# Kernel tuning notes

Hardware: AMD Instinct MI355X
Metric: run time of the kernel (lower is better)

The kernel has to match this reference:

```python
import jax, jax.numpy as jnp
import numpy as np

DT = 0.001  # fixed dt in SimplifiedSSM.forward
LN_EPS = 1e-5


def _layernorm(x, g, b):
    m = jnp.mean(x, axis=-1, keepdims=True)
    v = jnp.mean(jnp.square(x - m), axis=-1, keepdims=True)
    return (x - m) * jax.lax.rsqrt(v + LN_EPS) * g + b


def setup_inputs() -> dict:
    key = jax.random.key(0)
    ks = jax.random.split(key, 12)
    Bn, C, H, W = 8, 1024, 32, 32
    depth, S = 4, 128
    d = C
    inp = {
        "x": jax.random.normal(ks[0], (Bn, C, H, W), dtype=jnp.float32),
        # SSM params, stacked over depth. A scaled by 0.1 for numerical stability
        # of the length-1024 recurrence (same math, tamer eigenvalues).
        "A": 0.1 * jax.random.normal(ks[1], (depth, S, S), dtype=jnp.float32),
        "Bp": jax.random.normal(ks[2], (depth, S, d), dtype=jnp.float32),
        "Cp": jax.random.normal(ks[3], (depth, d, S), dtype=jnp.float32),
        "Dp": jax.random.normal(ks[4], (depth, d), dtype=jnp.float32),
        # Linear layers (PyTorch convention: y = x @ W.T + b)
        "Wi": jax.random.normal(ks[5], (depth, d, d), dtype=jnp.float32) / np.sqrt(d),
        "bi": jax.random.normal(ks[6], (depth, d), dtype=jnp.float32) * 0.01,
        "Wo": jax.random.normal(ks[7], (depth, d, d), dtype=jnp.float32) / np.sqrt(d),
        "bo": jax.random.normal(ks[8], (depth, d), dtype=jnp.float32) * 0.01,
        # LayerNorm affine params
        "gamma": jnp.ones((depth, d), dtype=jnp.float32),
        "beta": jnp.zeros((depth, d), dtype=jnp.float32),
    }
    return inp


def reference(x, A, Bp, Cp, Dp, Wi, bi, Wo, bo, gamma, beta):
    Bn, C, H, W = x.shape
    depth, S, _ = A.shape
    # b c h w -> b (h w) c
    seq = x.reshape(Bn, C, H * W).transpose(0, 2, 1)
    eye = jnp.eye(S, dtype=x.dtype)
    for i in range(depth):
        n = _layernorm(seq, gamma[i], beta[i])
        u = n @ Wi[i].T + bi[i]                       # (B, L, d)
        A_bar = eye + DT * A[i]                       # (S, S)
        ub = jnp.einsum('bld,sd->lbs', u, DT * Bp[i]) # (L, B, S)

        def step(h, ub_t):
            h = h @ A_bar.T + ub_t
            return h, h

        h0 = jnp.zeros((Bn, S), dtype=x.dtype)
        _, hs = jax.lax.scan(step, h0, ub)            # hs: (L, B, S)
        y = jnp.einsum('lbs,ds->bld', hs, Cp[i]) + u * Dp[i]
        seq = seq + y @ Wo[i].T + bo[i]
    return seq.transpose(0, 2, 1).reshape(Bn, C, H, W)
```

## Files before the change

### kernel.cpp

```cpp
#include <hip/hip_runtime.h>
#include <stdint.h>

#define DT_STEP 0.001f
#define LN_EPS  1e-5f
#define Bn      8
#define Lseq    1024
#define Dm      1024
#define Sn      128
#define DEPTH   4
#define Mrows   (Bn * Lseq)
#define Qc      32
#define NCHUNK  (Lseq / Qc)
#define NPOW    33

typedef short bf16x8 __attribute__((ext_vector_type(8)));
typedef float f32x4  __attribute__((ext_vector_type(4)));

__device__ __forceinline__ unsigned short f2bf(float f) {
    unsigned int u = __float_as_uint(f);
    u += 0x7fffu + ((u >> 16) & 1u);
    return (unsigned short)(u >> 16);
}

#define GLOAD_LDS16(gp, lp)                                                \
    __builtin_amdgcn_global_load_lds(                                      \
        (const __attribute__((address_space(1))) unsigned int*)(gp),       \
        (__attribute__((address_space(3))) unsigned int*)(lp), 16, 0, 0)

__global__ __launch_bounds__(256) void f2bf_kernel(const float* __restrict__ src,
                                                   unsigned short* __restrict__ dst,
                                                   int n) {
    int i = (blockIdx.x * 256 + threadIdx.x) * 4;
    if (i < n) {
        float4 v = *(const float4*)(src + i);
        ushort4 o;
        o.x = f2bf(v.x); o.y = f2bf(v.y); o.z = f2bf(v.z); o.w = f2bf(v.w);
        *(ushort4*)(dst + i) = o;
    }
}

__global__ __launch_bounds__(256) void convscale_kernel(const float* __restrict__ Wo,
                                                        const float* __restrict__ Dp,
                                                        unsigned short* __restrict__ dst) {
    int z = blockIdx.y;
    int i = (blockIdx.x * 256 + threadIdx.x) * 4;
    const float* S = Wo + (size_t)z * Dm * Dm;
    const float* dp = Dp + (size_t)z * Dm;
    float4 v = *(const float4*)(S + i);
    int c = i & (Dm - 1);
    float4 d = *(const float4*)(dp + c);
    ushort4 o;
    o.x = f2bf(v.x * d.x); o.y = f2bf(v.y * d.y);
    o.z = f2bf(v.z * d.z); o.w = f2bf(v.w * d.w);
    *(ushort4*)(dst + (size_t)z * Dm * Dm + i) = o;
}

__global__ __launch_bounds__(256) void transpose_f2bf(const float* __restrict__ src,
                                                      unsigned short* __restrict__ dst,
                                                      int R, int C) {
    __shared__ float t[32][33];
    int z = blockIdx.z;
    const float* S = src + (size_t)z * R * C;
    unsigned short* D = dst + (size_t)z * R * C;
    int r0 = blockIdx.y * 32, c0 = blockIdx.x * 32;
    int tx = threadIdx.x & 31, ty = threadIdx.x >> 5;
    for (int rr = ty; rr < 32; rr += 8)
        t[rr][tx] = S[(size_t)(r0 + rr) * C + c0 + tx];
    __syncthreads();
    for (int rr = ty; rr < 32; rr += 8)
        D[(size_t)(c0 + rr) * R + r0 + tx] = f2bf(t[tx][rr]);
}

__global__ __launch_bounds__(256) void c2dt_kernel(const float* __restrict__ Bp,
                                                   const float* __restrict__ bi,
                                                   float* __restrict__ c2dt) {
    int z = blockIdx.x, s = blockIdx.y;
    int tid = threadIdx.x;
    const float* br = Bp + ((size_t)z * Sn + s) * Dm;
    const float* bb = bi + (size_t)z * Dm;
    float4 v = *(const float4*)(br + tid * 4);
    float4 w = *(const float4*)(bb + tid * 4);
    float acc = v.x * w.x + v.y * w.y + v.z * w.z + v.w * w.w;
#pragma unroll
    for (int off = 32; off > 0; off >>= 1) acc += __shfl_down(acc, off, 64);
    __shared__ float red[4];
    if ((tid & 63) == 0) red[tid >> 6] = acc;
    __syncthreads();
    if (tid == 0) c2dt[z * Sn + s] = DT_STEP * (red[0] + red[1] + red[2] + red[3]);
}

__global__ __launch_bounds__(1024) void transpose_bll(const float* __restrict__ src,
                                                      float* __restrict__ dst) {
    __shared__ float tile[32][33];
    int b  = blockIdx.z;
    int i0 = blockIdx.y * 32, j0 = blockIdx.x * 32;
    int tx = threadIdx.x, ty = threadIdx.y;
    const float* S = src + (size_t)b * Dm * Lseq;
    float*       D = dst + (size_t)b * Dm * Lseq;
    tile[ty][tx] = S[(size_t)(j0 + ty) * 1024 + i0 + tx];
    __syncthreads();
    D[(size_t)(i0 + ty) * 1024 + j0 + tx] = tile[tx][ty];
}

__global__ __launch_bounds__(256) void ln_kernel(const float* __restrict__ x,
                                                 unsigned short* __restrict__ outp,
                                                 const float* __restrict__ g,
                                                 const float* __restrict__ bta) {
    int row = blockIdx.x;
    int tid = threadIdx.x;
    const float* xr = x + (size_t)row * Dm;
    float4 v = *(const float4*)(xr + tid * 4);
    float s  = v.x + v.y + v.z + v.w;
    float ss = v.x * v.x + v.y * v.y + v.z * v.z + v.w * v.w;
#pragma unroll
    for (int off = 32; off > 0; off >>= 1) {
        s  += __shfl_down(s, off, 64);
        ss += __shfl_down(ss, off, 64);
    }
    __shared__ float red[8];
    __shared__ float mv[2];
    int wave = tid >> 6, lane = tid & 63;
    if (lane == 0) { red[wave] = s; red[4 + wave] = ss; }
    __syncthreads();
    if (tid == 0) {
        float st  = red[0] + red[1] + red[2] + red[3];
        float sst = red[4] + red[5] + red[6] + red[7];
        float mean = st / (float)Dm;
        float var  = sst / (float)Dm - mean * mean;
        mv[0] = mean;
        mv[1] = rsqrtf(var + LN_EPS);
    }
    __syncthreads();
    float mean = mv[0], rstd = mv[1];
    int c = tid * 4;
    float4 gv = *(const float4*)(g + c);
    float4 bv = *(const float4*)(bta + c);
    ushort4 o;
    o.x = f2bf((v.x - mean) * rstd * gv.x + bv.x);
    o.y = f2bf((v.y - mean) * rstd * gv.y + bv.y);
    o.z = f2bf((v.z - mean) * rstd * gv.z + bv.z);
    o.w = f2bf((v.w - mean) * rstd * gv.w + bv.w);
    *(ushort4*)(outp + (size_t)row * Dm + c) = o;
}

__global__ __launch_bounds__(256) void gemm_bk64(
    const unsigned short* __restrict__ A1, int sA1,
    const unsigned short* __restrict__ A2, int sA2, int KA1,
    const unsigned short* __restrict__ B1, int sB1,
    const unsigned short* __restrict__ B2, int sB2,
    float* __restrict__ Cf, unsigned short* __restrict__ Ch,
    const float* __restrict__ bias1, const float* __restrict__ bias2,
    int ny, int N, int K, float scale, int mode,
    long batchA, long batchB, long batchC) {
    __shared__ __align__(16) unsigned short As[1024 * 8];
    __shared__ __align__(16) unsigned short Bs[1024 * 8];
    int flat = blockIdx.x;
    int rb = flat % ny, cb = flat / ny;
    int row0 = rb * 128, col0 = cb * 128;
    int z = blockIdx.y;
    int tid  = threadIdx.x;
    int wave = tid >> 6, lane = tid & 63;
    int wm = (wave >> 1) * 64, wn = (wave & 1) * 64;
    int lr = lane & 15, lq = lane >> 4;

    int rowS[4], kclS[4];
    unsigned short *Asl[4], *Bsl[4];
#pragma unroll
    for (int q = 0; q < 4; q++) {
        int s = tid + q * 256;
        rowS[q] = s >> 3;
        kclS[q] = (s & 7) ^ ((s >> 3) & 7);
        Asl[q] = &As[s * 8];
        Bsl[q] = &Bs[s * 8];
    }
    int aoff[4][2], boff[4][2];
#pragma unroll
    for (int i = 0; i < 4; i++)
#pragma unroll
        for (int h = 0; h < 2; h++) {
            int ra = wm + i * 16 + lr;
            aoff[i][h] = (ra * 8 + ((lq + 4 * h) ^ (ra & 7))) * 8;
            int rn = wn + i * 16 + lr;
            boff[i][h] = (rn * 8 + ((lq + 4 * h) ^ (rn & 7))) * 8;
        }

    const unsigned short* A1b = A1 + (size_t)z * batchA;
    const unsigned short* BfixBlk = nullptr;
    int sBfix = sB1;
    if (mode == 0) {
        if (col0 < N - 128) { BfixBlk = B1 + (size_t)col0 * sB1; sBfix = sB1; }
        else                { BfixBlk = B2;                      sBfix = sB2; }
    } else if (mode == 2) {
        BfixBlk = B1 + (size_t)z * batchB + (size_t)col0 * sB1;
        sBfix = sB1;
    }

    f32x4 acc[4][4];
#pragma unroll
    for (int i = 0; i < 4; i++)
#pragma unroll
        for (int j = 0; j < 4; j++) acc[i][j] = (f32x4){0.f, 0.f, 0.f, 0.f};

    for (int k0 = 0; k0 < K; k0 += 64) {
        const unsigned short *Ab, *Bb;
        int sa, sb, ko;
        if (mode == 1) {
            if (k0 < KA1) { Ab = A1; sa = sA1; Bb = B1 + (size_t)col0 * sB1; sb = sB1; ko = k0; }
            else          { Ab = A2; sa = sA2; Bb = B2 + (size_t)col0 * sB2; sb = sB2; ko = k0 - KA1; }
        } else {
            Ab = A1b; sa = sA1; Bb = BfixBlk; sb = sBfix; ko = k0;
        }
        const unsigned short* Abr = Ab + (size_t)row0 * sa + ko;
        const unsigned short* Bbr = Bb + ko;
        __syncthreads();
#pragma unroll
        for (int q = 0; q < 4; q++) {
            GLOAD_LDS16(Abr + (size_t)rowS[q] * sa + kclS[q] * 8, Asl[q]);
            GLOAD_LDS16(Bbr + (size_t)rowS[q] * sb + kclS[q] * 8, Bsl[q]);
        }
        __syncthreads();
#pragma unroll
        for (int h = 0; h < 2; h++) {
            bf16x8 af[4], bfr[4];
#pragma unroll
            for (int i = 0; i < 4; i++) af[i]  = *(const bf16x8*)&As[aoff[i][h]];
#pragma unroll
            for (int j = 0; j < 4; j++) bfr[j] = *(const bf16x8*)&Bs[boff[j][h]];
#pragma unroll
            for (int i = 0; i < 4; i++)
#pragma unroll
                for (int j = 0; j < 4; j++)
                    acc[i][j] = __builtin_amdgcn_mfma_f32_16x16x32_bf16(af[i], bfr[j],
                                                                       acc[i][j], 0, 0, 0);
        }
    }
#pragma unroll
    for (int i = 0; i < 4; i++) {
#pragma unroll
        for (int j = 0; j < 4; j++) {
#pragma unroll
            for (int r = 0; r < 4; r++) {
                int row = row0 + wm + i * 16 + lq * 4 + r;
                int col = col0 + wn + j * 16 + lr;
                float v = acc[i][j][r];
                if (mode == 0) {
                    int nu = N - 128;
                    if (col < nu) {
                        Ch[(size_t)row * nu + col] = f2bf(v + bias1[col]);
                    } else {
                        int cc = col - nu;
                        Cf[(size_t)row * 128 + cc] = v + bias2[cc];
                    }
                } else if (mode == 1) {
                    size_t idx = (size_t)row * N + col;
                    Cf[idx] = Cf[idx] + v + bias1[col];
                } else {
                    Ch[(size_t)z * batchC + (size_t)row * N + col] = f2bf(v * scale);
                }
            }
        }
    }
}

__global__ __launch_bounds__(128) void pow_init(const float* __restrict__ Amat,
                                                float* __restrict__ Pow) {
    int i = blockIdx.x;
    int s = blockIdx.y;
    int k = threadIdx.x;
    float eye = (s == k) ? 1.f : 0.f;
    size_t base = (size_t)i * NPOW * (Sn * Sn);
    Pow[base + (size_t)s * Sn + k] = eye;
    Pow[base + (size_t)(Sn * Sn) + (size_t)s * Sn + k] =
        eye + DT_STEP * Amat[(size_t)i * Sn * Sn + (size_t)s * Sn + k];
}

__global__ __launch_bounds__(256) void pow_mul(float* __restrict__ Pow, int m, int kmax) {
    int job = blockIdx.z;
    int i  = job / kmax;
    int kk = job % kmax + 1;
    const float* Pa = Pow + ((size_t)i * NPOW + m) * (Sn * Sn);
    const float* Pb = Pow + ((size_t)i * NPOW + kk) * (Sn * Sn);
    float*       Pc = Pow + ((size_t)i * NPOW + m + kk) * (Sn * Sn);
    int r0 = blockIdx.y * 64, c0 = blockIdx.x * 32;
    __shared__ float Asl[64 * 129];
    __shared__ float Bsl[128 * 32];
    int tx = threadIdx.x, ty = threadIdx.y;
    int tid = ty * 16 + tx;
    for (int idx = tid; idx < 64 * 128; idx += 256) {
        int r = idx >> 7, cc = idx & 127;
        Asl[r * 129 + cc] = Pa[(size_t)(r0 + r) * 128 + cc];
    }
    for (int idx = tid; idx < 128 * 32; idx += 256) {
        int r = idx >> 5, cc = idx & 31;
        Bsl[r * 32 + cc] = Pb[(size_t)r * 128 + c0 + cc];
    }
    __syncthreads();
    float acc[4][2] = {{0.f,0.f},{0.f,0.f},{0.f,0.f},{0.f,0.f}};
    for (int k = 0; k < 128; k++) {
        float b0 = Bsl[k * 32 + tx * 2];
        float b1 = Bsl[k * 32 + tx * 2 + 1];
#pragma unroll
        for (int r = 0; r < 4; r++) {
            float a = Asl[(ty * 4 + r) * 129 + k];
            acc[r][0] += a * b0;
            acc[r][1] += a * b1;
        }
    }
#pragma unroll
    for (int r = 0; r < 4; r++) {
        Pc[(size_t)(r0 + ty * 4 + r) * 128 + c0 + tx * 2]     = acc[r][0];
        Pc[(size_t)(r0 + ty * 4 + r) * 128 + c0 + tx * 2 + 1] = acc[r][1];
    }
}

__global__ __launch_bounds__(128) void local_scan(const float* __restrict__ ub,
                                                  float* __restrict__ hs,
                                                  const float* __restrict__ Abar) {
    int b = blockIdx.x / NCHUNK;
    int c = blockIdx.x % NCHUNK;
    int s = threadIdx.x;
    float arow[Sn];
#pragma unroll
    for (int k = 0; k < Sn; k += 4) {
        float4 v = *(const float4*)(Abar + (size_t)s * Sn + k);
        arow[k] = v.x; arow[k + 1] = v.y; arow[k + 2] = v.z; arow[k + 3] = v.w;
    }
    __shared__ __align__(16) float hsh[Sn];
    hsh[s] = 0.f;
    __syncthreads();
    size_t base = (size_t)(b * Lseq + c * Qc) * Sn + s;
    for (int t = 0; t < Qc; t++) {
        float ut = ub[base + (size_t)t * Sn];
        float a0 = 0.f, a1 = 0.f, a2 = 0.f, a3 = 0.f;
#pragma unroll
        for (int k = 0; k < Sn; k += 16) {
            float4 h0 = *(const float4*)&hsh[k];
            float4 h1 = *(const float4*)&hsh[k + 4];
            float4 h2 = *(const float4*)&hsh[k + 8];
            float4 h3 = *(const float4*)&hsh[k + 12];
            a0 += arow[k + 0] * h0.x + arow[k + 1] * h0.y + arow[k + 2] * h0.z + arow[k + 3] * h0.w;
            a1 += arow[k + 4] * h1.x + arow[k + 5] * h1.y + arow[k + 6] * h1.z + arow[k + 7] * h1.w;
            a2 += arow[k + 8] * h2.x + arow[k + 9] * h2.y + arow[k + 10] * h2.z + arow[k + 11] * h2.w;
            a3 += arow[k + 12] * h3.x + arow[k + 13] * h3.y + arow[k + 14] * h3.z + arow[k + 15] * h3.w;
        }
        float hv = ut + (a0 + a1) + (a2 + a3);
        hs[base + (size_t)t * Sn] = hv;
        __syncthreads();
        hsh[s] = hv;
        __syncthreads();
    }
}

__global__ __launch_bounds__(128) void carry_scan(const float* __restrict__ hs,
                                                  const float* __restrict__ AQ,
                                                  float* __restrict__ carry) {
    int b = blockIdx.x;
    int s = threadIdx.x;
    float le[NCHUNK];
#pragma unroll
    for (int c = 0; c < NCHUNK; c++)
        le[c] = hs[(size_t)(b * Lseq + c * Qc + Qc - 1) * Sn + s];
    float arow[Sn];
#pragma unroll
    for (int k = 0; k < Sn; k += 4) {
        float4 v = *(const float4*)(AQ + (size_t)s * Sn + k);
        arow[k] = v.x; arow[k + 1] = v.y; arow[k + 2] = v.z; arow[k + 3] = v.w;
    }
    __shared__ __align__(16) float csh[Sn];
    csh[s] = 0.f;
    __syncthreads();
    for (int c = 0; c < NCHUNK; c++) {
        carry[((size_t)b * NCHUNK + c) * Sn + s] = csh[s];
        float a0 = 0.f, a1 = 0.f, a2 = 0.f, a3 = 0.f;
#pragma unroll
        for (int k = 0; k < Sn; k += 16) {
            float4 h0 = *(const float4*)&csh[k];
            float4 h1 = *(const float4*)&csh[k + 4];
            float4 h2 = *(const float4*)&csh[k + 8];
            float4 h3 = *(const float4*)&csh[k + 12];
            a0 += arow[k + 0] * h0.x + arow[k + 1] * h0.y + arow[k + 2] * h0.z + arow[k + 3] * h0.w;
            a1 += arow[k + 4] * h1.x + arow[k + 5] * h1.y + arow[k + 6] * h1.z + arow[k + 7] * h1.w;
            a2 += arow[k + 8] * h2.x + arow[k + 9] * h2.y + arow[k + 10] * h2.z + arow[k + 11] * h2.w;
            a3 += arow[k + 12] * h3.x + arow[k + 13] * h3.y + arow[k + 14] * h3.z + arow[k + 15] * h3.w;
        }
        float cv = le[c] + (a0 + a1) + (a2 + a3);
        __syncthreads();
        csh[s] = cv;
        __syncthreads();
    }
}

__global__ __launch_bounds__(256) void fixup_scan(const float* __restrict__ hs,
                                                  unsigned short* __restrict__ hs_bf,
                                                  const float* __restrict__ PowLayer,
                                                  const float* __restrict__ carry) {
    int t = blockIdx.x;
    int c = blockIdx.y;
    const float* P = PowLayer + (size_t)(t + 1) * (Sn * Sn);
    __shared__ float Pl[Sn * 65];
    __shared__ float cl[Bn * Sn];
    int tid = threadIdx.x;
    for (int idx = tid; idx < Bn * Sn; idx += 256)
        cl[idx] = carry[((size_t)(idx >> 7) * NCHUNK + c) * Sn + (idx & 127)];
    int s = tid & 127, bh = tid >> 7;
    float acc[4] = {0.f, 0.f, 0.f, 0.f};
    for (int kh = 0; kh < 2; kh++) {
        __syncthreads();
        for (int idx = tid; idx < Sn * 64; idx += 256) {
            int r = idx >> 6, kk = idx & 63;
            Pl[r * 65 + kk] = P[(size_t)r * Sn + kh * 64 + kk];
        }
        __syncthreads();
        for (int kk = 0; kk < 64; kk++) {
            float pw = Pl[s * 65 + kk];
            int kg = kh * 64 + kk;
#pragma unroll
            for (int j = 0; j < 4; j++)
                acc[j] += pw * cl[(bh * 4 + j) * Sn + kg];
        }
    }
#pragma unroll
    for (int j = 0; j < 4; j++) {
        int bb = bh * 4 + j;
        size_t rowi = (size_t)(bb * Lseq + c * Qc + t) * Sn + s;
        hs_bf[rowi] = f2bf(hs[rowi] + acc[j]);
    }
}

extern "C" void kernel_launch(void* const* d_in, const int* in_sizes, int n_in,
                              void* d_out, int out_size, void* d_ws, size_t ws_size,
                              hipStream_t stream) {
    const float* x     = (const float*)d_in[0];
    const float* Am    = (const float*)d_in[1];
    const float* Bp    = (const float*)d_in[2];
    const float* Cp    = (const float*)d_in[3];
    const float* Dp    = (const float*)d_in[4];
    const float* Wi    = (const float*)d_in[5];
    const float* bi    = (const float*)d_in[6];
    const float* Wo    = (const float*)d_in[7];
    const float* bo    = (const float*)d_in[8];
    const float* gamma = (const float*)d_in[9];
    const float* beta  = (const float*)d_in[10];
    float* out = (float*)d_out;
    (void)in_sizes; (void)n_in; (void)out_size; (void)ws_size;

    char* ws = (char*)d_ws;
    float*          seq   = (float*)(ws + (size_t)0);
    unsigned short* nbuf  = (unsigned short*)(ws + (size_t)33554432);
    unsigned short* WiTh  = (unsigned short*)(ws + (size_t)33554432);
    unsigned short* Woh   = (unsigned short*)(ws + (size_t)41943040);
    unsigned short* u     = (unsigned short*)(ws + (size_t)50331648);
    float*          ub    = (float*)(ws + (size_t)67108864);
    float*          hs    = (float*)(ws + (size_t)71303168);
    unsigned short* hs_bf = (unsigned short*)(ws + (size_t)75497472);
    float*          Pow   = (float*)(ws + (size_t)77594624);
    float*          carry = (float*)(ws + (size_t)86245376);
    unsigned short* Wih   = (unsigned short*)(ws + (size_t)86376448);
    unsigned short* Wo2h  = (unsigned short*)(ws + (size_t)94765056);
    unsigned short* Bph   = (unsigned short*)(ws + (size_t)103153664);
    unsigned short* CpTh  = (unsigned short*)(ws + (size_t)104202240);
    unsigned short* M2h   = (unsigned short*)(ws + (size_t)105250816);
    unsigned short* W3h   = (unsigned short*)(ws + (size_t)106299392);
    float*          c2dt  = (float*)(ws + (size_t)107347968);

    const long WW = (long)Dm * Dm;
    const long SW = (long)Sn * Dm;

    hipLaunchKernelGGL(f2bf_kernel, dim3(DEPTH * WW / 1024), dim3(256), 0, stream,
                       Wi, Wih, DEPTH * (int)WW);
    hipLaunchKernelGGL(f2bf_kernel, dim3(DEPTH * WW / 1024), dim3(256), 0, stream,
                       Wo, Woh, DEPTH * (int)WW);
    hipLaunchKernelGGL(f2bf_kernel, dim3(DEPTH * SW / 1024), dim3(256), 0, stream,
                       Bp, Bph, DEPTH * (int)SW);
    hipLaunchKernelGGL(convscale_kernel, dim3(WW / 1024, DEPTH), dim3(256), 0, stream,
                       Wo, Dp, Wo2h);
    hipLaunchKernelGGL(transpose_f2bf, dim3(32, 32, DEPTH), dim3(256), 0, stream,
                       Wi, WiTh, Dm, Dm);
    hipLaunchKernelGGL(transpose_f2bf, dim3(4, 32, DEPTH), dim3(256), 0, stream,
                       Cp, CpTh, Dm, Sn);
    hipLaunchKernelGGL(c2dt_kernel, dim3(DEPTH, Sn), dim3(256), 0, stream, Bp, bi, c2dt);

    hipLaunchKernelGGL(gemm_bk64, dim3(8, DEPTH), dim3(256), 0, stream,
                       Bph, Dm, (const unsigned short*)nullptr, 0, 0,
                       WiTh, Dm, (const unsigned short*)nullptr, 0,
                       (float*)nullptr, M2h, (const float*)nullptr, (const float*)nullptr,
                       1, Dm, Dm, DT_STEP, 2, SW, WW, SW);
    hipLaunchKernelGGL(gemm_bk64, dim3(8, DEPTH), dim3(256), 0, stream,
                       Woh, Dm, (const unsigned short*)nullptr, 0, 0,
                       CpTh, Dm, (const unsigned short*)nullptr, 0,
                       (float*)nullptr, W3h, (const float*)nullptr, (const float*)nullptr,
                       8, Sn, Dm, 1.f, 2, WW, SW, SW);

    hipLaunchKernelGGL(transpose_bll, dim3(32, 32, Bn), dim3(32, 32), 0, stream, x, seq);

    hipLaunchKernelGGL(pow_init, dim3(DEPTH, Sn), dim3(Sn), 0, stream, Am, Pow);
    for (int m = 1; m < Qc; m <<= 1) {
        hipLaunchKernelGGL(pow_mul, dim3(4, 2, DEPTH * m), dim3(16, 16), 0, stream,
                           Pow, m, m);
    }

    for (int i = 0; i < DEPTH; i++) {
        const unsigned short* Wi_i  = Wih  + (size_t)i * WW;
        const unsigned short* Wo2_i = Wo2h + (size_t)i * WW;
        const unsigned short* M2_i  = M2h  + (size_t)i * SW;
        const unsigned short* W3_i  = W3h  + (size_t)i * SW;
        const float* PowL = Pow + (size_t)i * NPOW * (Sn * Sn);

        hipLaunchKernelGGL(ln_kernel, dim3(Mrows), dim3(256), 0, stream,
                           seq, nbuf, gamma + i * Dm, beta + i * Dm);
        hipLaunchKernelGGL(gemm_bk64, dim3(9 * 64, 1), dim3(256), 0, stream,
                           nbuf, Dm, (const unsigned short*)nullptr, 0, 0,
                           Wi_i, Dm, M2_i, Dm,
                           ub, u, bi + i * Dm, c2dt + i * Sn,
                           64, Dm + Sn, Dm, 1.f, 0, 0, 0, 0);
        hipLaunchKernelGGL(local_scan, dim3(Bn * NCHUNK), dim3(Sn), 0, stream,
                           ub, hs, PowL + (size_t)1 * Sn * Sn);
        hipLaunchKernelGGL(carry_scan, dim3(Bn), dim3(Sn), 0, stream,
                           hs, PowL + (size_t)Qc * Sn * Sn, carry);
        hipLaunchKernelGGL(fixup_scan, dim3(Qc, NCHUNK), dim3(256), 0, stream,
                           hs, hs_bf, PowL, carry);
        hipLaunchKernelGGL(gemm_bk64, dim3(8 * 64, 1), dim3(256), 0, stream,
                           hs_bf, Sn, u, Dm, Sn,
                           W3_i, Sn, Wo2_i, Dm,
                           seq, (unsigned short*)nullptr, bo + i * Dm, (const float*)nullptr,
                           64, Dm, Dm + Sn, 1.f, 1, 0, 0, 0);
    }

    hipLaunchKernelGGL(transpose_bll, dim3(32, 32, Bn), dim3(32, 32), 0, stream, seq, out);
}
```

Measured before the change: 855.1 us.

## Double-buffer LDS tiles in bf16 GEMM to overlap global loads with MFMA

Doubles the shared-memory A/B tile buffers and restructures the K loop so the next tile's global-to-LDS loads are issued before computing on the current tile. Explicit s_waitcnt vmcnt/lgkmcnt plus s_barrier inline asm replace the two __syncthreads per iteration. The goal is to hide global memory latency behind the matrix-core work. In exchange, LDS use doubles to 64KB per block, which may reduce occupancy, and correctness now relies on hand-counted wait counts.

Result: slower. 952.2 us (+11.4%).

```diff
diff --git a/kernel.cpp b/kernel.cpp
--- a/kernel.cpp
+++ b/kernel.cpp
@@ -152,8 +152,8 @@
     const float* __restrict__ bias1, const float* __restrict__ bias2,
     int ny, int N, int K, float scale, int mode,
     long batchA, long batchB, long batchC) {
-    __shared__ __align__(16) unsigned short As[1024 * 8];
-    __shared__ __align__(16) unsigned short Bs[1024 * 8];
+    __shared__ __align__(16) unsigned short As[2][1024 * 8];
+    __shared__ __align__(16) unsigned short Bs[2][1024 * 8];
     int flat = blockIdx.x;
     int rb = flat % ny, cb = flat / ny;
     int row0 = rb * 128, col0 = cb * 128;
@@ -163,15 +163,13 @@
     int wm = (wave >> 1) * 64, wn = (wave & 1) * 64;
     int lr = lane & 15, lq = lane >> 4;
 
-    int rowS[4], kclS[4];
-    unsigned short *Asl[4], *Bsl[4];
+    int rowS[4], kclS[4], slotOff[4];
 #pragma unroll
     for (int q = 0; q < 4; q++) {
         int s = tid + q * 256;
         rowS[q] = s >> 3;
         kclS[q] = (s & 7) ^ ((s >> 3) & 7);
-        Asl[q] = &As[s * 8];
-        Bsl[q] = &Bs[s * 8];
+        slotOff[q] = s * 8;
     }
     int aoff[4][2], boff[4][2];
 #pragma unroll
@@ -195,13 +193,8 @@
         sBfix = sB1;
     }
 
-    f32x4 acc[4][4];
-#pragma unroll
-    for (int i = 0; i < 4; i++)
-#pragma unroll
-        for (int j = 0; j < 4; j++) acc[i][j] = (f32x4){0.f, 0.f, 0.f, 0.f};
-
-    for (int k0 = 0; k0 < K; k0 += 64) {
+    auto issue = [&](int kt, int buf) {
+        int k0 = kt * 64;
         const unsigned short *Ab, *Bb;
         int sa, sb, ko;
         if (mode == 1) {
@@ -212,20 +205,27 @@
         }
         const unsigned short* Abr = Ab + (size_t)row0 * sa + ko;
         const unsigned short* Bbr = Bb + ko;
-        __syncthreads();
 #pragma unroll
         for (int q = 0; q < 4; q++) {
-            GLOAD_LDS16(Abr + (size_t)rowS[q] * sa + kclS[q] * 8, Asl[q]);
-            GLOAD_LDS16(Bbr + (size_t)rowS[q] * sb + kclS[q] * 8, Bsl[q]);
-        }
-        __syncthreads();
+            GLOAD_LDS16(Abr + (size_t)rowS[q] * sa + kclS[q] * 8, &As[buf][slotOff[q]]);
+            GLOAD_LDS16(Bbr + (size_t)rowS[q] * sb + kclS[q] * 8, &Bs[buf][slotOff[q]]);
+        }
+    };
+
+    f32x4 acc[4][4];
+#pragma unroll
+    for (int i = 0; i < 4; i++)
+#pragma unroll
+        for (int j = 0; j < 4; j++) acc[i][j] = (f32x4){0.f, 0.f, 0.f, 0.f};
+
+    auto compute = [&](int buf) {
 #pragma unroll
         for (int h = 0; h < 2; h++) {
             bf16x8 af[4], bfr[4];
 #pragma unroll
-            for (int i = 0; i < 4; i++) af[i]  = *(const bf16x8*)&As[aoff[i][h]];
-#pragma unroll
-            for (int j = 0; j < 4; j++) bfr[j] = *(const bf16x8*)&Bs[boff[j][h]];
+            for (int i = 0; i < 4; i++) af[i]  = *(const bf16x8*)&As[buf][aoff[i][h]];
+#pragma unroll
+            for (int j = 0; j < 4; j++) bfr[j] = *(const bf16x8*)&Bs[buf][boff[j][h]];
 #pragma unroll
             for (int i = 0; i < 4; i++)
 #pragma unroll
@@ -233,7 +233,20 @@
                     acc[i][j] = __builtin_amdgcn_mfma_f32_16x16x32_bf16(af[i], bfr[j],
                                                                        acc[i][j], 0, 0, 0);
         }
-    }
+    };
+
+    int niter = K >> 6;
+    issue(0, 0);
+    int it = 0;
+    for (; it + 1 < niter; it++) {
+        issue(it + 1, (it + 1) & 1);
+        asm volatile("s_waitcnt vmcnt(8)\n\ts_barrier" ::: "memory");
+        compute(it & 1);
+        asm volatile("s_waitcnt lgkmcnt(0)\n\ts_barrier" ::: "memory");
+    }
+    asm volatile("s_waitcnt vmcnt(0)\n\ts_barrier" ::: "memory");
+    compute(it & 1);
+
 #pragma unroll
     for (int i = 0; i < 4; i++) {
 #pragma unroll
```

## Use 8-wave GEMM blocks and batch four chunks per fixup_scan block

Applied to the files above, without the earlier changes.

The 128x128 GEMM tile is now computed by 512 threads (8 waves, each 64x32) instead of 256 threads (4 waves, each 64x64). This halves per-thread accumulators and loads to raise latency hiding and occupancy, at the cost of more B-fragment LDS reads per MFMA. Separately, fixup_scan now handles four chunks per block, so each loaded power-matrix tile in LDS is reused across four carries, cutting redundant P loads. It quarters that kernel's block count and uses more shared memory per block.

Measured after the change: 812.2 us. -5.0%, faster.

```diff
diff --git a/kernel.cpp b/kernel.cpp
--- a/kernel.cpp
+++ b/kernel.cpp
@@ -143,7 +143,7 @@
     *(ushort4*)(outp + (size_t)row * Dm + c) = o;
 }
 
-__global__ __launch_bounds__(256) void gemm_bk64(
+__global__ __launch_bounds__(512) void gemm_bk64(
     const unsigned short* __restrict__ A1, int sA1,
     const unsigned short* __restrict__ A2, int sA2, int KA1,
     const unsigned short* __restrict__ B1, int sB1,
@@ -160,28 +160,31 @@
     int z = blockIdx.y;
     int tid  = threadIdx.x;
     int wave = tid >> 6, lane = tid & 63;
-    int wm = (wave >> 1) * 64, wn = (wave & 1) * 64;
+    int wm = (wave & 1) * 64, wn = (wave >> 1) * 32;
     int lr = lane & 15, lq = lane >> 4;
 
-    int rowS[4], kclS[4];
-    unsigned short *Asl[4], *Bsl[4];
-#pragma unroll
-    for (int q = 0; q < 4; q++) {
-        int s = tid + q * 256;
+    int rowS[2], kclS[2], slotOff[2];
+#pragma unroll
+    for (int q = 0; q < 2; q++) {
+        int s = tid + q * 512;
         rowS[q] = s >> 3;
         kclS[q] = (s & 7) ^ ((s >> 3) & 7);
-        Asl[q] = &As[s * 8];
-        Bsl[q] = &Bs[s * 8];
-    }
-    int aoff[4][2], boff[4][2];
+        slotOff[q] = s * 8;
+    }
+    int aoff[4][2], boff[2][2];
 #pragma unroll
     for (int i = 0; i < 4; i++)
 #pragma unroll
         for (int h = 0; h < 2; h++) {
             int ra = wm + i * 16 + lr;
             aoff[i][h] = (ra * 8 + ((lq + 4 * h) ^ (ra & 7))) * 8;
-            int rn = wn + i * 16 + lr;
-            boff[i][h] = (rn * 8 + ((lq + 4 * h) ^ (rn & 7))) * 8;
+        }
+#pragma unroll
+    for (int j = 0; j < 2; j++)
+#pragma unroll
+        for (int h = 0; h < 2; h++) {
+            int rn = wn + j * 16 + lr;
+            boff[j][h] = (rn * 8 + ((lq + 4 * h) ^ (rn & 7))) * 8;
         }
 
     const unsigned short* A1b = A1 + (size_t)z * batchA;
@@ -195,11 +198,11 @@
         sBfix = sB1;
     }
 
-    f32x4 acc[4][4];
+    f32x4 acc[4][2];
 #pragma unroll
     for (int i = 0; i < 4; i++)
 #pragma unroll
-        for (int j = 0; j < 4; j++) acc[i][j] = (f32x4){0.f, 0.f, 0.f, 0.f};
+        for (int j = 0; j < 2; j++) acc[i][j] = (f32x4){0.f, 0.f, 0.f, 0.f};
 
     for (int k0 = 0; k0 < K; k0 += 64) {
         const unsigned short *Ab, *Bb;
@@ -214,22 +217,22 @@
         const unsigned short* Bbr = Bb + ko;
         __syncthreads();
 #pragma unroll
-        for (int q = 0; q < 4; q++) {
-            GLOAD_LDS16(Abr + (size_t)rowS[q] * sa + kclS[q] * 8, Asl[q]);
-            GLOAD_LDS16(Bbr + (size_t)rowS[q] * sb + kclS[q] * 8, Bsl[q]);
+        for (int q = 0; q < 2; q++) {
+            GLOAD_LDS16(Abr + (size_t)rowS[q] * sa + kclS[q] * 8, &As[slotOff[q]]);
+            GLOAD_LDS16(Bbr + (size_t)rowS[q] * sb + kclS[q] * 8, &Bs[slotOff[q]]);
         }
         __syncthreads();
 #pragma unroll
         for (int h = 0; h < 2; h++) {
-            bf16x8 af[4], bfr[4];
+            bf16x8 af[4], bfr[2];
 #pragma unroll
             for (int i = 0; i < 4; i++) af[i]  = *(const bf16x8*)&As[aoff[i][h]];
 #pragma unroll
-            for (int j = 0; j < 4; j++) bfr[j] = *(const bf16x8*)&Bs[boff[j][h]];
+            for (int j = 0; j < 2; j++) bfr[j] = *(const bf16x8*)&Bs[boff[j][h]];
 #pragma unroll
             for (int i = 0; i < 4; i++)
 #pragma unroll
-                for (int j = 0; j < 4; j++)
+                for (int j = 0; j < 2; j++)
                     acc[i][j] = __builtin_amdgcn_mfma_f32_16x16x32_bf16(af[i], bfr[j],
                                                                        acc[i][j], 0, 0, 0);
         }
@@ -237,7 +240,7 @@
 #pragma unroll
     for (int i = 0; i < 4; i++) {
 #pragma unroll
-        for (int j = 0; j < 4; j++) {
+        for (int j = 0; j < 2; j++) {
 #pragma unroll
             for (int r = 0; r < 4; r++) {
                 int row = row0 + wm + i * 16 + lq * 4 + r;
@@ -394,16 +397,22 @@
                                                   unsigned short* __restrict__ hs_bf,
                                                   const float* __restrict__ PowLayer,
                                                   const float* __restrict__ carry) {
-    int t = blockIdx.x;
-    int c = blockIdx.y;
+    int t  = blockIdx.x;
+    int c4 = blockIdx.y;
     const float* P = PowLayer + (size_t)(t + 1) * (Sn * Sn);
     __shared__ float Pl[Sn * 65];
-    __shared__ float cl[Bn * Sn];
+    __shared__ float cl[4][Bn * Sn];
     int tid = threadIdx.x;
-    for (int idx = tid; idx < Bn * Sn; idx += 256)
-        cl[idx] = carry[((size_t)(idx >> 7) * NCHUNK + c) * Sn + (idx & 127)];
+#pragma unroll
+    for (int cc = 0; cc < 4; cc++)
+        for (int idx = tid; idx < Bn * Sn; idx += 256)
+            cl[cc][idx] = carry[((size_t)(idx >> 7) * NCHUNK + (c4 * 4 + cc)) * Sn + (idx & 127)];
     int s = tid & 127, bh = tid >> 7;
-    float acc[4] = {0.f, 0.f, 0.f, 0.f};
+    float acc[4][4];
+#pragma unroll
+    for (int cc = 0; cc < 4; cc++)
+#pragma unroll
+        for (int j = 0; j < 4; j++) acc[cc][j] = 0.f;
     for (int kh = 0; kh < 2; kh++) {
         __syncthreads();
         for (int idx = tid; idx < Sn * 64; idx += 256) {
@@ -415,15 +424,21 @@
             float pw = Pl[s * 65 + kk];
             int kg = kh * 64 + kk;
 #pragma unroll
-            for (int j = 0; j < 4; j++)
-                acc[j] += pw * cl[(bh * 4 + j) * Sn + kg];
-        }
-    }
-#pragma unroll
-    for (int j = 0; j < 4; j++) {
-        int bb = bh * 4 + j;
-        size_t rowi = (size_t)(bb * Lseq + c * Qc + t) * Sn + s;
-        hs_bf[rowi] = f2bf(hs[rowi] + acc[j]);
+            for (int cc = 0; cc < 4; cc++)
+#pragma unroll
+                for (int j = 0; j < 4; j++)
+                    acc[cc][j] += pw * cl[cc][(bh * 4 + j) * Sn + kg];
+        }
+    }
+#pragma unroll
+    for (int cc = 0; cc < 4; cc++) {
+        int c = c4 * 4 + cc;
+#pragma unroll
+        for (int j = 0; j < 4; j++) {
+            int bb = bh * 4 + j;
+            size_t rowi = (size_t)(bb * Lseq + c * Qc + t) * Sn + s;
+            hs_bf[rowi] = f2bf(hs[rowi] + acc[cc][j]);
+        }
     }
 }
 
@@ -480,12 +495,12 @@
                        Cp, CpTh, Dm, Sn);
     hipLaunchKernelGGL(c2dt_kernel, dim3(DEPTH, Sn), dim3(256), 0, stream, Bp, bi, c2dt);
 
-    hipLaunchKernelGGL(gemm_bk64, dim3(8, DEPTH), dim3(256), 0, stream,
+    hipLaunchKernelGGL(gemm_bk64, dim3(8, DEPTH), dim3(512), 0, stream,
                        Bph, Dm, (const unsigned short*)nullptr, 0, 0,
                        WiTh, Dm, (const unsigned short*)nullptr, 0,
                        (float*)nullptr, M2h, (const float*)nullptr, (const float*)nullptr,
                        1, Dm, Dm, DT_STEP, 2, SW, WW, SW);
-    hipLaunchKernelGGL(gemm_bk64, dim3(8, DEPTH), dim3(256), 0, stream,
+    hipLaunchKernelGGL(gemm_bk64, dim3(8, DEPTH), dim3(512), 0, stream,
                        Woh, Dm, (const unsigned short*)nullptr, 0, 0,
                        CpTh, Dm, (const unsigned short*)nullptr, 0,
                        (float*)nullptr, W3h, (const float*)nullptr, (const float*)nullptr,
@@ -508,7 +523,7 @@
 
         hipLaunchKernelGGL(ln_kernel, dim3(Mrows), dim3(256), 0, stream,
                            seq, nbuf, gamma + i * Dm, beta + i * Dm);
-        hipLaunchKernelGGL(gemm_bk64, dim3(9 * 64, 1), dim3(256), 0, stream,
+        hipLaunchKernelGGL(gemm_bk64, dim3(9 * 64, 1), dim3(512), 0, stream,
                            nbuf, Dm, (const unsigned short*)nullptr, 0, 0,
                            Wi_i, Dm, M2_i, Dm,
                            ub, u, bi + i * Dm, c2dt + i * Sn,
@@ -517,9 +532,9 @@
                            ub, hs, PowL + (size_t)1 * Sn * Sn);
         hipLaunchKernelGGL(carry_scan, dim3(Bn), dim3(Sn), 0, stream,
                            hs, PowL + (size_t)Qc * Sn * Sn, carry);
-        hipLaunchKernelGGL(fixup_scan, dim3(Qc, NCHUNK), dim3(256), 0, stream,
+        hipLaunchKernelGGL(fixup_scan, dim3(Qc, NCHUNK / 4), dim3(256), 0, stream,
                            hs, hs_bf, PowL, carry);
-        hipLaunchKernelGGL(gemm_bk64, dim3(8 * 64, 1), dim3(256), 0, stream,
+        hipLaunchKernelGGL(gemm_bk64, dim3(8 * 64, 1), dim3(512), 0, stream,
                            hs_bf, Sn, u, Dm, Sn,
                            W3_i, Sn, Wo2_i, Dm,
                            seq, (unsigned short*)nullptr, bo + i * Dm, (const float*)nullptr,
```
